# Kernel tuning notes

Measured on AMD Instinct MI355X. Metric: run time of the kernel, lower is better.

Reference implementation:

```python
import jax, jax.numpy as jnp
import numpy as np

B, T, NODES, DEG = 16, 50, 62, 8
IN, C, H, NC, K = 64, 128, 256, 3, 5
G = B * T            # num_graphs
N = G * NODES        # total nodes
E = G * NODES * DEG  # total edges (before self loops)


def setup_inputs() -> dict:
    key = jax.random.key(0)
    ks = jax.random.split(key, 12)
    # random within-graph edges, PyG-batched with node offsets
    rng = np.random.RandomState(0)
    src = rng.randint(0, NODES, size=(G, NODES * DEG))
    dst = rng.randint(0, NODES, size=(G, NODES * DEG))
    off = (np.arange(G) * NODES)[:, None]
    edge_index = jnp.asarray(np.stack([(src + off).ravel(), (dst + off).ravel()]), dtype=jnp.int32)

    def glorot(k, shape, fan_in):
        return jax.random.normal(k, shape, jnp.float32) / np.sqrt(fan_in)

    return {
        "x": jax.random.normal(ks[0], (N, IN), jnp.float32),
        "edge_index": edge_index,
        "edge_attr": jax.random.normal(ks[1], (E, 1), jnp.float32),
        "W_l": glorot(ks[2], (IN, C), IN), "b_l": jnp.zeros((C,), jnp.float32),
        "W_r": glorot(ks[3], (IN, C), IN), "b_r": jnp.zeros((C,), jnp.float32),
        "W_e": glorot(ks[4], (1, C), 1),
        "att": glorot(ks[5], (C,), C),
        "bias_out": jnp.zeros((C,), jnp.float32),
        "W_ih": glorot(ks[6], (3 * H, C), C), "W_hh": glorot(ks[7], (3 * H, H), H),
        "b_ih": jnp.zeros((3 * H,), jnp.float32), "b_hh": jnp.zeros((3 * H,), jnp.float32),
        "W1": glorot(ks[8], (H, H // 2), H), "b1": jnp.zeros((H // 2,), jnp.float32),
        "W2": glorot(ks[9], (H // 2, NC), H // 2), "b2": jnp.zeros((NC,), jnp.float32),
    }


def _forward(x, edge_index, edge_attr, W_l, b_l, W_r, b_r, W_e, att, bias_out,
             W_ih, W_hh, b_ih, b_hh, W1, b1, W2, b2):
    n = x.shape[0]
    src, dst = edge_index[0], edge_index[1]

    # --- GATv2Conv: add self loops with edge_attr fill_value='mean' (PyG default) ---
    sum_attr = jax.ops.segment_sum(edge_attr, dst, num_segments=n)
    cnt = jax.ops.segment_sum(jnp.ones_like(dst, jnp.float32), dst, num_segments=n)
    loop_attr = sum_attr / jnp.clip(cnt, 1.0)[:, None]
    ar = jnp.arange(n, dtype=src.dtype)
    src2 = jnp.concatenate([src, ar])
    dst2 = jnp.concatenate([dst, ar])
    ea = jnp.concatenate([edge_attr, loop_attr], axis=0)

    xl = x @ W_l + b_l          # source-side transform
    xr = x @ W_r + b_r          # target-side transform
    ee = ea @ W_e               # edge embedding (lin_edge, bias=False)

    m = xl[src2] + xr[dst2] + ee                # [E2, C]
    e = jax.nn.leaky_relu(m, 0.2) @ att         # [E2]
    # scatter-softmax over incoming edges per target node (self loops => no empty segs)
    emax = jax.ops.segment_max(e, dst2, num_segments=n)
    ez = jnp.exp(e - emax[dst2])
    den = jax.ops.segment_sum(ez, dst2, num_segments=n)
    alpha = ez / den[dst2]                      # [E2]
    h_sp = jax.ops.segment_sum(alpha[:, None] * xl[src2], dst2, num_segments=n) + bias_out

    # --- mean pool per graph (uniform graph size => reshape) ---
    g = h_sp.reshape(G, NODES, C).mean(axis=1).reshape(B, T, C)

    # --- GRU (PyTorch gate order r, z, n) ---
    def step(h, xt):
        gx = xt @ W_ih.T + b_ih
        gh = h @ W_hh.T + b_hh
        xr_, xz, xn = jnp.split(gx, 3, axis=-1)
        hr, hz, hn = jnp.split(gh, 3, axis=-1)
        r = jax.nn.sigmoid(xr_ + hr)
        z = jax.nn.sigmoid(xz + hz)
        nn_ = jnp.tanh(xn + r * hn)
        h2 = (1.0 - z) * nn_ + z * h
        return h2, h2

    h0 = jnp.zeros((B, H), g.dtype)
    _, hs = jax.lax.scan(step, h0, jnp.swapaxes(g, 0, 1))  # [T,B,H]
    gru_out = jnp.swapaxes(hs, 0, 1)                       # [B,T,H]

    # --- classifier (dropout inactive at eval) ---
    scores = jax.nn.relu(gru_out @ W1 + b1) @ W2 + b2      # [B,T,NC]

    # --- top-k over time per class, then mean over k ---
    vals, idx = jax.lax.top_k(jnp.swapaxes(scores, 1, 2), K)  # [B,NC,K]
    return vals.mean(axis=-1), jnp.swapaxes(idx, 1, 2)        # [B,NC], [B,K,NC]


def reference(x, edge_index, edge_attr, W_l, b_l, W_r, b_r, W_e, att, bias_out,
              W_ih, W_hh, b_ih, b_hh, W1, b1, W2, b2):
    return _forward(x, edge_index, edge_attr, W_l, b_l, W_r, b_r, W_e, att, bias_out,
                    W_ih, W_hh, b_ih, b_hh, W1, b1, W2, b2)
```

## Files before the change

### kernel.cpp

```cpp
#include <hip/hip_runtime.h>
#include <math.h>

#define NNODES 62
#define NDEG 8
#define NGRAPH 800
#define NB 16
#define NT 50
#define NIN 64
#define NCH 128
#define NH 256
#define NCLS 3
#define NTOPK 5
#define NSL 8
#define EPG (NNODES*NDEG)
#define E2G (EPG + NNODES)
#define NTOTAL (NGRAPH*NNODES)
#define ETOTAL (NGRAPH*EPG)

__launch_bounds__(256, 2)
__global__ void k_xrl(const float* __restrict__ x,
                      const float* __restrict__ W_r, const float* __restrict__ b_r,
                      const float* __restrict__ W_l, const float* __restrict__ b_l,
                      float* __restrict__ xr, float* __restrict__ xl) {
    __shared__ __align__(16) float x_s[64 * NIN];
    __shared__ __align__(16) float wr_s[NIN * NCH];
    __shared__ __align__(16) float wl_s[NIN * NCH];
    const int blk = blockIdx.x;
    const int tid = threadIdx.x;
    const int base_v = blk * 64;

    {
        const float4* src = reinterpret_cast<const float4*>(x + (size_t)base_v * NIN);
        float4* dst = reinterpret_cast<float4*>(x_s);
        for (int i = tid; i < 64 * NIN / 4; i += 256) dst[i] = src[i];
        const float4* sr = reinterpret_cast<const float4*>(W_r);
        const float4* sl = reinterpret_cast<const float4*>(W_l);
        float4* dr = reinterpret_cast<float4*>(wr_s);
        float4* dl = reinterpret_cast<float4*>(wl_s);
        for (int i = tid; i < NIN * NCH / 4; i += 256) { dr[i] = sr[i]; dl[i] = sl[i]; }
    }
    __syncthreads();

    const int c4 = (tid & 31) * 4;
    const int ng = tid >> 5;
    float4 aR[8], aL[8];
    float4 br4 = *reinterpret_cast<const float4*>(b_r + c4);
    float4 bl4 = *reinterpret_cast<const float4*>(b_l + c4);
    #pragma unroll
    for (int j = 0; j < 8; ++j) { aR[j] = br4; aL[j] = bl4; }

    const float* xs = x_s + (ng * 8) * NIN;
    for (int k4 = 0; k4 < NIN; k4 += 4) {
        float4 xv[8];
        #pragma unroll
        for (int j = 0; j < 8; ++j)
            xv[j] = *reinterpret_cast<const float4*>(&xs[j * NIN + k4]);
        #pragma unroll
        for (int kk = 0; kk < 4; ++kk) {
            float4 wr = *reinterpret_cast<const float4*>(&wr_s[(k4 + kk) * NCH + c4]);
            float4 wl = *reinterpret_cast<const float4*>(&wl_s[(k4 + kk) * NCH + c4]);
            #pragma unroll
            for (int j = 0; j < 8; ++j) {
                float xk = (kk == 0) ? xv[j].x : (kk == 1) ? xv[j].y
                         : (kk == 2) ? xv[j].z : xv[j].w;
                aR[j].x += xk * wr.x; aR[j].y += xk * wr.y;
                aR[j].z += xk * wr.z; aR[j].w += xk * wr.w;
                aL[j].x += xk * wl.x; aL[j].y += xk * wl.y;
                aL[j].z += xk * wl.z; aL[j].w += xk * wl.w;
            }
        }
    }
    #pragma unroll
    for (int j = 0; j < 8; ++j) {
        int v = base_v + ng * 8 + j;
        *reinterpret_cast<float4*>(xr + (size_t)v * NCH + c4) = aR[j];
        *reinterpret_cast<float4*>(xl + (size_t)v * NCH + c4) = aL[j];
    }
}

__global__ void k_transpose(const float* __restrict__ src, float* __restrict__ dst,
                            int rows, int cols) {
    int idx = blockIdx.x * blockDim.x + threadIdx.x;
    if (idx >= rows * cols) return;
    int r = idx / cols;
    int c = idx - r * cols;
    dst[c * rows + r] = src[idx];
}

__launch_bounds__(256, 4)
__global__ void k_gat(const int* __restrict__ ei, const float* __restrict__ eattr,
                      const float* __restrict__ W_e, const float* __restrict__ att,
                      const float* __restrict__ bias_out,
                      const float* __restrict__ xr_all, const float* __restrict__ xl_all,
                      float* __restrict__ g_all) {
    __shared__ __align__(16) float xl_s[NNODES * NCH];
    __shared__ unsigned short csr_src[E2G];
    __shared__ float csr_attr[E2G];
    __shared__ float csr_e[E2G];
    __shared__ unsigned short off_s[NNODES + 2];
    __shared__ unsigned cur_s[NNODES];
    __shared__ unsigned cnt_s[NNODES];
    __shared__ float asum_s[NNODES];
    __shared__ float la_s[NNODES];
    __shared__ float gacc_s[4 * NCH];

    const int g = blockIdx.x;
    const int tid = threadIdx.x;
    const int base_e = g * EPG;
    const int base_n = g * NNODES;

    for (int v = tid; v < NNODES; v += 256) { asum_s[v] = 0.f; cnt_s[v] = 0u; cur_s[v] = 0u; }
    {
        const float4* src = reinterpret_cast<const float4*>(xl_all + (size_t)base_n * NCH);
        float4* dst = reinterpret_cast<float4*>(xl_s);
        for (int i = tid; i < NNODES * NCH / 4; i += 256) dst[i] = src[i];
    }
    int s0 = -1, d0 = 0, s1 = -1, d1 = 0;
    float a0 = 0.f, a1 = 0.f;
    {
        int j0 = tid * 2, j1 = tid * 2 + 1;
        if (j0 < EPG) { s0 = ei[base_e + j0] - base_n; d0 = ei[ETOTAL + base_e + j0] - base_n; a0 = eattr[base_e + j0]; }
        if (j1 < EPG) { s1 = ei[base_e + j1] - base_n; d1 = ei[ETOTAL + base_e + j1] - base_n; a1 = eattr[base_e + j1]; }
    }
    __syncthreads();

    if (s0 >= 0) { atomicAdd(&cnt_s[d0], 1u); atomicAdd(&asum_s[d0], a0); }
    if (s1 >= 0) { atomicAdd(&cnt_s[d1], 1u); atomicAdd(&asum_s[d1], a1); }
    __syncthreads();

    if (tid < 64) {
        unsigned val = (tid < NNODES) ? (cnt_s[tid] + 1u) : 0u;
        unsigned xsc = val;
        #pragma unroll
        for (int dlt = 1; dlt < 64; dlt <<= 1) {
            unsigned o = __shfl_up(xsc, dlt, 64);
            if (tid >= dlt) xsc += o;
        }
        if (tid < NNODES) {
            off_s[tid] = (unsigned short)(xsc - val);
            la_s[tid] = asum_s[tid] / fmaxf((float)cnt_s[tid], 1.f);
        }
        if (tid == NNODES - 1) off_s[NNODES] = (unsigned short)xsc;
    }
    __syncthreads();

    if (s0 >= 0) { int sl = off_s[d0] + (int)atomicAdd(&cur_s[d0], 1u); csr_src[sl] = (unsigned short)s0; csr_attr[sl] = a0; }
    if (s1 >= 0) { int sl = off_s[d1] + (int)atomicAdd(&cur_s[d1], 1u); csr_src[sl] = (unsigned short)s1; csr_attr[sl] = a1; }
    if (tid < NNODES) { int sl = off_s[tid + 1] - 1; csr_src[sl] = (unsigned short)tid; csr_attr[sl] = la_s[tid]; }
    __syncthreads();

    const int wave = tid >> 6;
    const int lane = tid & 63;
    const int sub = lane & 15;
    const int gslot = wave * 4 + (lane >> 4);
    const int cb = sub * 8;

    float we0[8], at0[8];
    #pragma unroll
    for (int i = 0; i < 8; ++i) { we0[i] = W_e[cb + i]; at0[i] = att[cb + i]; }

    float acc[8];
    #pragma unroll
    for (int i = 0; i < 8; ++i) acc[i] = 0.f;

    for (int v = gslot; v < NNODES; v += 16) {
        const float* xrp = xr_all + (size_t)(base_n + v) * NCH + cb;
        float4 xr0 = *reinterpret_cast<const float4*>(xrp);
        float4 xr1 = *reinterpret_cast<const float4*>(xrp + 4);
        const int lo = off_s[v], hi = off_s[v + 1];
        float m = -INFINITY, ssum = 0.f;
        for (int sl = lo; sl < hi; ++sl) {
            int src = csr_src[sl];
            float a = csr_attr[sl];
            float4 x0 = *reinterpret_cast<const float4*>(&xl_s[src * NCH + cb]);
            float4 x1 = *reinterpret_cast<const float4*>(&xl_s[src * NCH + cb + 4]);
            float m0, t = 0.f;
            m0 = x0.x + xr0.x + a * we0[0]; t += (m0 >= 0.f ? m0 : 0.2f * m0) * at0[0];
            m0 = x0.y + xr0.y + a * we0[1]; t += (m0 >= 0.f ? m0 : 0.2f * m0) * at0[1];
            m0 = x0.z + xr0.z + a * we0[2]; t += (m0 >= 0.f ? m0 : 0.2f * m0) * at0[2];
            m0 = x0.w + xr0.w + a * we0[3]; t += (m0 >= 0.f ? m0 : 0.2f * m0) * at0[3];
            m0 = x1.x + xr1.x + a * we0[4]; t += (m0 >= 0.f ? m0 : 0.2f * m0) * at0[4];
            m0 = x1.y + xr1.y + a * we0[5]; t += (m0 >= 0.f ? m0 : 0.2f * m0) * at0[5];
            m0 = x1.z + xr1.z + a * we0[6]; t += (m0 >= 0.f ? m0 : 0.2f * m0) * at0[6];
            m0 = x1.w + xr1.w + a * we0[7]; t += (m0 >= 0.f ? m0 : 0.2f * m0) * at0[7];
            t += __shfl_xor(t, 1, 64);
            t += __shfl_xor(t, 2, 64);
            t += __shfl_xor(t, 4, 64);
            t += __shfl_xor(t, 8, 64);
            if (sub == 0) csr_e[sl] = t;
            float mn = fmaxf(m, t);
            ssum = ssum * __expf(m - mn) + __expf(t - mn);
            m = mn;
        }
        float inv = 1.f / ssum;
        for (int sl = lo; sl < hi; ++sl) {
            int src = csr_src[sl];
            float al = __expf(csr_e[sl] - m) * inv;
            float4 x0 = *reinterpret_cast<const float4*>(&xl_s[src * NCH + cb]);
            float4 x1 = *reinterpret_cast<const float4*>(&xl_s[src * NCH + cb + 4]);
            acc[0] += al * x0.x; acc[1] += al * x0.y;
            acc[2] += al * x0.z; acc[3] += al * x0.w;
            acc[4] += al * x1.x; acc[5] += al * x1.y;
            acc[6] += al * x1.z; acc[7] += al * x1.w;
        }
    }
    #pragma unroll
    for (int i = 0; i < 8; ++i) {
        acc[i] += __shfl_xor(acc[i], 16, 64);
        acc[i] += __shfl_xor(acc[i], 32, 64);
    }
    if ((lane >> 4) == 0) {
        *reinterpret_cast<float4*>(&gacc_s[wave * NCH + cb]) =
            make_float4(acc[0], acc[1], acc[2], acc[3]);
        *reinterpret_cast<float4*>(&gacc_s[wave * NCH + cb + 4]) =
            make_float4(acc[4], acc[5], acc[6], acc[7]);
    }
    __syncthreads();

    for (int c = tid; c < NCH; c += 256) {
        float v = (gacc_s[c] + gacc_s[NCH + c] + gacc_s[2 * NCH + c] + gacc_s[3 * NCH + c])
                      * (1.f / NNODES) + bias_out[c];
        g_all[(size_t)g * NCH + c] = v;
    }
}

__global__ void k_gx(const float* __restrict__ g_all, const float* __restrict__ W_ihT,
                     const float* __restrict__ b_ih, const float* __restrict__ b_hh,
                     float* __restrict__ gx_all, unsigned long long* __restrict__ h_pub) {
    if (blockIdx.x < 32)
        h_pub[(size_t)blockIdx.x * 256 + threadIdx.x] = 0ull;
    int idx = blockIdx.x * blockDim.x + threadIdx.x;
    if (idx >= NGRAPH * 3 * NH) return;
    int gi = idx / (3 * NH);
    int o = idx - gi * (3 * NH);
    float acc = b_ih[o] + (o < 2 * NH ? b_hh[o] : 0.f);
    const float* grow = g_all + (size_t)gi * NCH;
    for (int c = 0; c < NCH; ++c) acc += grow[c] * W_ihT[c * (3 * NH) + o];
    gx_all[idx] = acc;
}

__launch_bounds__(256)
__global__ void k_gru(const float* __restrict__ gx_all, const float* __restrict__ W_hh,
                      const float* __restrict__ b_hh, float* __restrict__ h_all,
                      unsigned long long* __restrict__ h_pub) {
    __shared__ __align__(16) float h_s[NH];
    __shared__ float gh_s[96];
    __shared__ float gx_s[2][96];

    const int bid = blockIdx.x;
    const int b = bid >> 3;
    const int s = bid & 7;
    const int tid = threadIdx.x;
    const int wv = tid >> 6;
    const int g = tid >> 1;
    const int l = tid & 1;

    float4 Wv[32];
    if (tid < 192) {
        int row = (g / 32) * NH + 32 * s + (g & 31);
        const float* wr = W_hh + (size_t)row * NH + 128 * l;
        #pragma unroll
        for (int j = 0; j < 32; ++j) Wv[j] = *reinterpret_cast<const float4*>(wr + 4 * j);
    }
    const float bhn = (tid < 32) ? b_hh[2 * NH + 32 * s + tid] : 0.f;
    const int own_lo = 32 * s, own_hi = own_lo + 32;

    for (int i = tid; i < NH; i += 256) h_s[i] = 0.f;
    if (wv == 3) {
        int i = tid - 192;
        int o = (i < 32) ? (32 * s + i) : (NH + 32 * s + (i - 32));
        gx_s[0][i] = gx_all[(size_t)(b * NT) * (3 * NH) + o];
        if (i < 32) gx_s[0][i + 64] = gx_all[(size_t)(b * NT) * (3 * NH) + 2 * NH + 32 * s + i];
    }
    __syncthreads();

    for (int t = 0; t < NT; ++t) {
        const int par = (t + 1) & 1;
        if (wv == 3) {
            int i = tid - 192;
            if (t + 1 < NT) {
                size_t base = (size_t)(b * NT + t + 1) * (3 * NH);
                int o = (i < 32) ? (32 * s + i) : (NH + 32 * s + (i - 32));
                gx_s[par][i] = gx_all[base + o];
                if (i < 32) gx_s[par][i + 64] = gx_all[base + 2 * NH + 32 * s + i];
            }
        } else {
            float a0 = 0.f, a1 = 0.f, a2 = 0.f, a3 = 0.f;
            #pragma unroll
            for (int j = 0; j < 32; ++j) {
                float4 hv = *reinterpret_cast<const float4*>(&h_s[128 * l + 4 * j]);
                float4 w = Wv[j];
                a0 += w.x * hv.x; a1 += w.y * hv.y; a2 += w.z * hv.z; a3 += w.w * hv.w;
            }
            float acc = (a0 + a1) + (a2 + a3);
            acc += __shfl_xor(acc, 1, 64);
            if (l == 0) gh_s[g] = acc;
        }
        __syncthreads();

        if (tid < 32) {
            const float* gx = gx_s[t & 1];
            float r = 1.f / (1.f + expf(-(gx[tid] + gh_s[tid])));
            float z = 1.f / (1.f + expf(-(gx[32 + tid] + gh_s[32 + tid])));
            float n = tanhf(gx[64 + tid] + r * (gh_s[64 + tid] + bhn));
            int o = own_lo + tid;
            float hv = (1.f - z) * n + z * h_s[o];
            h_all[(size_t)(b * NT + t) * NH + o] = hv;
            unsigned long long w = ((unsigned long long)(unsigned)(t + 1) << 32)
                                 | (unsigned long long)__float_as_uint(hv);
            __hip_atomic_store(&h_pub[((size_t)b * 2 + par) * NH + o], w,
                               __ATOMIC_RELAXED, __HIP_MEMORY_SCOPE_AGENT);
            h_s[o] = hv;
        }
        if (tid < own_lo || tid >= own_hi) {
            const unsigned long long* p = &h_pub[((size_t)b * 2 + par) * NH + tid];
            unsigned long long w;
            const unsigned target = (unsigned)(t + 1);
            while ((unsigned)((w = __hip_atomic_load(p, __ATOMIC_RELAXED,
                                                     __HIP_MEMORY_SCOPE_AGENT)) >> 32) != target)
                ;
            h_s[tid] = __uint_as_float((unsigned)w);
        }
        __syncthreads();
    }
}

__launch_bounds__(128)
__global__ void k_cls(const float* __restrict__ h_all,
                      const float* __restrict__ W1, const float* __restrict__ b1,
                      const float* __restrict__ W2, const float* __restrict__ b2,
                      float* __restrict__ sc_all) {
    __shared__ float h_s[NH];
    __shared__ float s1_s[NH / 2];
    const int bt = blockIdx.x;
    const int tid = threadIdx.x;
    h_s[tid] = h_all[(size_t)bt * NH + tid];
    h_s[tid + 128] = h_all[(size_t)bt * NH + tid + 128];
    __syncthreads();
    float acc = b1[tid];
    #pragma unroll 8
    for (int k = 0; k < NH; ++k) acc += h_s[k] * W1[k * (NH / 2) + tid];
    s1_s[tid] = fmaxf(acc, 0.f);
    __syncthreads();
    if (tid < NCLS) {
        float a = b2[tid];
        for (int k = 0; k < NH / 2; ++k) a += s1_s[k] * W2[k * NCLS + tid];
        sc_all[bt * NCLS + tid] = a;
    }
}

__global__ void k_topk(const float* __restrict__ sc_all, float* __restrict__ out) {
    int tid = threadIdx.x;
    if (tid >= NB * NCLS) return;
    int b = tid / NCLS;
    int c = tid - b * NCLS;
    float vals[NT];
    for (int t = 0; t < NT; ++t) vals[t] = sc_all[(b * NT + t) * NCLS + c];
    float sum = 0.f;
    for (int k = 0; k < NTOPK; ++k) {
        float best = -INFINITY; int bi = 0;
        for (int t = 0; t < NT; ++t) {
            if (vals[t] > best) { best = vals[t]; bi = t; }
        }
        vals[bi] = -INFINITY;
        sum += best;
        out[NB * NCLS + b * (NTOPK * NCLS) + k * NCLS + c] = (float)bi;
    }
    out[b * NCLS + c] = sum * (1.f / NTOPK);
}

extern "C" void kernel_launch(void* const* d_in, const int* in_sizes, int n_in,
                              void* d_out, int out_size, void* d_ws, size_t ws_size,
                              hipStream_t stream) {
    const float* x        = (const float*)d_in[0];
    const int*   ei       = (const int*)  d_in[1];
    const float* eattr    = (const float*)d_in[2];
    const float* W_l      = (const float*)d_in[3];
    const float* b_l      = (const float*)d_in[4];
    const float* W_r      = (const float*)d_in[5];
    const float* b_r      = (const float*)d_in[6];
    const float* W_e      = (const float*)d_in[7];
    const float* att      = (const float*)d_in[8];
    const float* bias_out = (const float*)d_in[9];
    const float* W_ih     = (const float*)d_in[10];
    const float* W_hh     = (const float*)d_in[11];
    const float* b_ih     = (const float*)d_in[12];
    const float* b_hh     = (const float*)d_in[13];
    const float* W1       = (const float*)d_in[14];
    const float* b1       = (const float*)d_in[15];
    const float* W2       = (const float*)d_in[16];
    const float* b2       = (const float*)d_in[17];
    float* out = (float*)d_out;

    float* ws = (float*)d_ws;
    float* xr_all = ws;
    float* xl_all = xr_all + (size_t)NTOTAL * NCH;
    float* g_all  = xl_all + (size_t)NTOTAL * NCH;
    float* gx_all = g_all + NGRAPH * NCH;
    float* W_ihT  = gx_all + NGRAPH * 3 * NH;
    float* h_all  = W_ihT + NCH * 3 * NH;
    float* sc_all = h_all + (size_t)NGRAPH * NH;
    unsigned long long* h_pub = (unsigned long long*)xr_all;

    k_xrl<<<NTOTAL / 64, 256, 0, stream>>>(x, W_r, b_r, W_l, b_l, xr_all, xl_all);
    k_transpose<<<(3 * NH * NCH + 255) / 256, 256, 0, stream>>>(W_ih, W_ihT, 3 * NH, NCH);
    k_gat<<<NGRAPH, 256, 0, stream>>>(ei, eattr, W_e, att, bias_out, xr_all, xl_all, g_all);
    k_gx<<<(NGRAPH * 3 * NH + 255) / 256, 256, 0, stream>>>(g_all, W_ihT, b_ih, b_hh, gx_all, h_pub);
    k_gru<<<NB * NSL, 256, 0, stream>>>(gx_all, W_hh, b_hh, h_all, h_pub);
    k_cls<<<NB * NT, 128, 0, stream>>>(h_all, W1, b1, W2, b2, sc_all);
    k_topk<<<1, 64, 0, stream>>>(sc_all, out);
}
```

Measured before the change: 227.4 us.

## Fuse node projections and W_ih transpose into GAT kernel; split GRU across more blocks

Each GAT block now computes the xl/xr projections for its own graph directly into padded shared memory, using 512 threads. This removes the separate projection kernel and the global round-trip of the xr/xl arrays. The W_ih transpose is folded into extra trailing blocks of the same launch, and the GRU recurrence is spread over 16 slices per batch with 4 lanes per gate row instead of 8 slices. The fused kernel reloads W_r/W_l into shared memory in every block and uses a large shared footprint, which limits occupancy to one block. The finer GRU split also adds more cross-block spin synchronization per step.

```diff
diff --git a/kernel.cpp b/kernel.cpp
--- a/kernel.cpp
+++ b/kernel.cpp
@@ -11,121 +11,116 @@
 #define NH 256
 #define NCLS 3
 #define NTOPK 5
-#define NSL 8
+#define NSL 16
 #define EPG (NNODES*NDEG)
 #define E2G (EPG + NNODES)
 #define NTOTAL (NGRAPH*NNODES)
 #define ETOTAL (NGRAPH*EPG)
-
-__launch_bounds__(256, 2)
-__global__ void k_xrl(const float* __restrict__ x,
+#define TBLK 97
+#define WST (NIN*NCH + 4)
+#define XST 68
+#define XLST 132
+
+__launch_bounds__(512, 1)
+__global__ void k_gat(const float* __restrict__ x, const int* __restrict__ ei,
+                      const float* __restrict__ eattr,
                       const float* __restrict__ W_r, const float* __restrict__ b_r,
                       const float* __restrict__ W_l, const float* __restrict__ b_l,
-                      float* __restrict__ xr, float* __restrict__ xl) {
-    __shared__ __align__(16) float x_s[64 * NIN];
-    __shared__ __align__(16) float wr_s[NIN * NCH];
-    __shared__ __align__(16) float wl_s[NIN * NCH];
-    const int blk = blockIdx.x;
-    const int tid = threadIdx.x;
-    const int base_v = blk * 64;
-
-    {
-        const float4* src = reinterpret_cast<const float4*>(x + (size_t)base_v * NIN);
-        float4* dst = reinterpret_cast<float4*>(x_s);
-        for (int i = tid; i < 64 * NIN / 4; i += 256) dst[i] = src[i];
-        const float4* sr = reinterpret_cast<const float4*>(W_r);
-        const float4* sl = reinterpret_cast<const float4*>(W_l);
-        float4* dr = reinterpret_cast<float4*>(wr_s);
-        float4* dl = reinterpret_cast<float4*>(wl_s);
-        for (int i = tid; i < NIN * NCH / 4; i += 256) { dr[i] = sr[i]; dl[i] = sl[i]; }
-    }
-    __syncthreads();
-
-    const int c4 = (tid & 31) * 4;
-    const int ng = tid >> 5;
-    float4 aR[8], aL[8];
-    float4 br4 = *reinterpret_cast<const float4*>(b_r + c4);
-    float4 bl4 = *reinterpret_cast<const float4*>(b_l + c4);
-    #pragma unroll
-    for (int j = 0; j < 8; ++j) { aR[j] = br4; aL[j] = bl4; }
-
-    const float* xs = x_s + (ng * 8) * NIN;
-    for (int k4 = 0; k4 < NIN; k4 += 4) {
-        float4 xv[8];
-        #pragma unroll
-        for (int j = 0; j < 8; ++j)
-            xv[j] = *reinterpret_cast<const float4*>(&xs[j * NIN + k4]);
-        #pragma unroll
-        for (int kk = 0; kk < 4; ++kk) {
-            float4 wr = *reinterpret_cast<const float4*>(&wr_s[(k4 + kk) * NCH + c4]);
-            float4 wl = *reinterpret_cast<const float4*>(&wl_s[(k4 + kk) * NCH + c4]);
-            #pragma unroll
-            for (int j = 0; j < 8; ++j) {
-                float xk = (kk == 0) ? xv[j].x : (kk == 1) ? xv[j].y
-                         : (kk == 2) ? xv[j].z : xv[j].w;
-                aR[j].x += xk * wr.x; aR[j].y += xk * wr.y;
-                aR[j].z += xk * wr.z; aR[j].w += xk * wr.w;
-                aL[j].x += xk * wl.x; aL[j].y += xk * wl.y;
-                aL[j].z += xk * wl.z; aL[j].w += xk * wl.w;
-            }
-        }
-    }
-    #pragma unroll
-    for (int j = 0; j < 8; ++j) {
-        int v = base_v + ng * 8 + j;
-        *reinterpret_cast<float4*>(xr + (size_t)v * NCH + c4) = aR[j];
-        *reinterpret_cast<float4*>(xl + (size_t)v * NCH + c4) = aL[j];
-    }
-}
-
-__global__ void k_transpose(const float* __restrict__ src, float* __restrict__ dst,
-                            int rows, int cols) {
-    int idx = blockIdx.x * blockDim.x + threadIdx.x;
-    if (idx >= rows * cols) return;
-    int r = idx / cols;
-    int c = idx - r * cols;
-    dst[c * rows + r] = src[idx];
-}
-
-__launch_bounds__(256, 4)
-__global__ void k_gat(const int* __restrict__ ei, const float* __restrict__ eattr,
                       const float* __restrict__ W_e, const float* __restrict__ att,
                       const float* __restrict__ bias_out,
-                      const float* __restrict__ xr_all, const float* __restrict__ xl_all,
+                      const float* __restrict__ W_ih, float* __restrict__ W_ihT,
                       float* __restrict__ g_all) {
-    __shared__ __align__(16) float xl_s[NNODES * NCH];
-    __shared__ unsigned short csr_src[E2G];
+    __shared__ __align__(16) float w_s[2 * WST];
+    __shared__ __align__(16) float x_s[64 * XST];
+    __shared__ __align__(16) float xl_s[NNODES * XLST];
+    __shared__ __align__(16) float xr_s[NNODES * XLST];
     __shared__ float csr_attr[E2G];
     __shared__ float csr_e[E2G];
+    __shared__ unsigned short csr_src[E2G];
     __shared__ unsigned short off_s[NNODES + 2];
     __shared__ unsigned cur_s[NNODES];
     __shared__ unsigned cnt_s[NNODES];
     __shared__ float asum_s[NNODES];
     __shared__ float la_s[NNODES];
-    __shared__ float gacc_s[4 * NCH];
+    __shared__ float gacc_s[8 * NCH];
 
     const int g = blockIdx.x;
     const int tid = threadIdx.x;
+    if (g >= NGRAPH) {
+        for (int idx = (g - NGRAPH) * 512 + tid; idx < 3 * NH * NCH; idx += TBLK * 512) {
+            int r = idx / NCH, c = idx - r * NCH;
+            W_ihT[c * (3 * NH) + r] = W_ih[idx];
+        }
+        return;
+    }
     const int base_e = g * EPG;
     const int base_n = g * NNODES;
 
-    for (int v = tid; v < NNODES; v += 256) { asum_s[v] = 0.f; cnt_s[v] = 0u; cur_s[v] = 0u; }
+    for (int v = tid; v < NNODES; v += 512) { asum_s[v] = 0.f; cnt_s[v] = 0u; cur_s[v] = 0u; }
+    int s0 = -1, d0 = 0; float a0e = 0.f;
+    if (tid < EPG) {
+        s0 = ei[base_e + tid] - base_n;
+        d0 = ei[ETOTAL + base_e + tid] - base_n;
+        a0e = eattr[base_e + tid];
+    }
     {
-        const float4* src = reinterpret_cast<const float4*>(xl_all + (size_t)base_n * NCH);
-        float4* dst = reinterpret_cast<float4*>(xl_s);
-        for (int i = tid; i < NNODES * NCH / 4; i += 256) dst[i] = src[i];
-    }
-    int s0 = -1, d0 = 0, s1 = -1, d1 = 0;
-    float a0 = 0.f, a1 = 0.f;
-    {
-        int j0 = tid * 2, j1 = tid * 2 + 1;
-        if (j0 < EPG) { s0 = ei[base_e + j0] - base_n; d0 = ei[ETOTAL + base_e + j0] - base_n; a0 = eattr[base_e + j0]; }
-        if (j1 < EPG) { s1 = ei[base_e + j1] - base_n; d1 = ei[ETOTAL + base_e + j1] - base_n; a1 = eattr[base_e + j1]; }
-    }
-    __syncthreads();
-
-    if (s0 >= 0) { atomicAdd(&cnt_s[d0], 1u); atomicAdd(&asum_s[d0], a0); }
-    if (s1 >= 0) { atomicAdd(&cnt_s[d1], 1u); atomicAdd(&asum_s[d1], a1); }
+        float4* dr = reinterpret_cast<float4*>(w_s);
+        float4* dl = reinterpret_cast<float4*>(w_s + WST);
+        const float4* sr = reinterpret_cast<const float4*>(W_r);
+        const float4* sl = reinterpret_cast<const float4*>(W_l);
+        for (int i = tid; i < NIN * NCH / 4; i += 512) { dr[i] = sr[i]; dl[i] = sl[i]; }
+        for (int i = tid; i < NNODES * (NIN / 4); i += 512) {
+            int r = i >> 4, c = i & 15;
+            reinterpret_cast<float4*>(&x_s[r * XST])[c] =
+                reinterpret_cast<const float4*>(x + (size_t)(base_n + r) * NIN)[c];
+        }
+    }
+    __syncthreads();
+    if (s0 >= 0) { atomicAdd(&cnt_s[d0], 1u); atomicAdd(&asum_s[d0], a0e); }
+
+    if (tid < 256) {
+        const int mat = tid >> 7;
+        const int u = tid & 127;
+        const int cg = u & 15;
+        const int ng = u >> 4;
+        const int cb2 = cg * 8;
+        const float* Ws = w_s + mat * WST;
+        const float* bb = mat ? b_l : b_r;
+        float4 bv0 = *reinterpret_cast<const float4*>(bb + cb2);
+        float4 bv1 = *reinterpret_cast<const float4*>(bb + cb2 + 4);
+        float4 A0[8], A1[8];
+        #pragma unroll
+        for (int j = 0; j < 8; ++j) { A0[j] = bv0; A1[j] = bv1; }
+        for (int k4 = 0; k4 < NIN; k4 += 4) {
+            float4 xv[8];
+            #pragma unroll
+            for (int j = 0; j < 8; ++j)
+                xv[j] = *reinterpret_cast<const float4*>(&x_s[(ng * 8 + j) * XST + k4]);
+            #pragma unroll
+            for (int kk = 0; kk < 4; ++kk) {
+                float4 w0 = *reinterpret_cast<const float4*>(&Ws[(k4 + kk) * NCH + cb2]);
+                float4 w1 = *reinterpret_cast<const float4*>(&Ws[(k4 + kk) * NCH + cb2 + 4]);
+                #pragma unroll
+                for (int j = 0; j < 8; ++j) {
+                    float xk = (kk == 0) ? xv[j].x : (kk == 1) ? xv[j].y
+                             : (kk == 2) ? xv[j].z : xv[j].w;
+                    A0[j].x += xk * w0.x; A0[j].y += xk * w0.y;
+                    A0[j].z += xk * w0.z; A0[j].w += xk * w0.w;
+                    A1[j].x += xk * w1.x; A1[j].y += xk * w1.y;
+                    A1[j].z += xk * w1.z; A1[j].w += xk * w1.w;
+                }
+            }
+        }
+        float* dst = mat ? xl_s : xr_s;
+        #pragma unroll
+        for (int j = 0; j < 8; ++j) {
+            int v = ng * 8 + j;
+            if (v < NNODES) {
+                *reinterpret_cast<float4*>(&dst[v * XLST + cb2]) = A0[j];
+                *reinterpret_cast<float4*>(&dst[v * XLST + cb2 + 4]) = A1[j];
+            }
+        }
+    }
     __syncthreads();
 
     if (tid < 64) {
@@ -143,10 +138,14 @@
         if (tid == NNODES - 1) off_s[NNODES] = (unsigned short)xsc;
     }
     __syncthreads();
-
-    if (s0 >= 0) { int sl = off_s[d0] + (int)atomicAdd(&cur_s[d0], 1u); csr_src[sl] = (unsigned short)s0; csr_attr[sl] = a0; }
-    if (s1 >= 0) { int sl = off_s[d1] + (int)atomicAdd(&cur_s[d1], 1u); csr_src[sl] = (unsigned short)s1; csr_attr[sl] = a1; }
-    if (tid < NNODES) { int sl = off_s[tid + 1] - 1; csr_src[sl] = (unsigned short)tid; csr_attr[sl] = la_s[tid]; }
+    if (s0 >= 0) {
+        int sl = off_s[d0] + (int)atomicAdd(&cur_s[d0], 1u);
+        csr_src[sl] = (unsigned short)s0; csr_attr[sl] = a0e;
+    }
+    if (tid < NNODES) {
+        int sl = off_s[tid + 1] - 1;
+        csr_src[sl] = (unsigned short)tid; csr_attr[sl] = la_s[tid];
+    }
     __syncthreads();
 
     const int wave = tid >> 6;
@@ -154,35 +153,32 @@
     const int sub = lane & 15;
     const int gslot = wave * 4 + (lane >> 4);
     const int cb = sub * 8;
-
     float we0[8], at0[8];
     #pragma unroll
     for (int i = 0; i < 8; ++i) { we0[i] = W_e[cb + i]; at0[i] = att[cb + i]; }
-
     float acc[8];
     #pragma unroll
     for (int i = 0; i < 8; ++i) acc[i] = 0.f;
 
-    for (int v = gslot; v < NNODES; v += 16) {
-        const float* xrp = xr_all + (size_t)(base_n + v) * NCH + cb;
-        float4 xr0 = *reinterpret_cast<const float4*>(xrp);
-        float4 xr1 = *reinterpret_cast<const float4*>(xrp + 4);
+    for (int v = gslot; v < NNODES; v += 32) {
+        float4 xr0 = *reinterpret_cast<const float4*>(&xr_s[v * XLST + cb]);
+        float4 xr1 = *reinterpret_cast<const float4*>(&xr_s[v * XLST + cb + 4]);
         const int lo = off_s[v], hi = off_s[v + 1];
         float m = -INFINITY, ssum = 0.f;
         for (int sl = lo; sl < hi; ++sl) {
             int src = csr_src[sl];
             float a = csr_attr[sl];
-            float4 x0 = *reinterpret_cast<const float4*>(&xl_s[src * NCH + cb]);
-            float4 x1 = *reinterpret_cast<const float4*>(&xl_s[src * NCH + cb + 4]);
-            float m0, t = 0.f;
-            m0 = x0.x + xr0.x + a * we0[0]; t += (m0 >= 0.f ? m0 : 0.2f * m0) * at0[0];
-            m0 = x0.y + xr0.y + a * we0[1]; t += (m0 >= 0.f ? m0 : 0.2f * m0) * at0[1];
-            m0 = x0.z + xr0.z + a * we0[2]; t += (m0 >= 0.f ? m0 : 0.2f * m0) * at0[2];
-            m0 = x0.w + xr0.w + a * we0[3]; t += (m0 >= 0.f ? m0 : 0.2f * m0) * at0[3];
-            m0 = x1.x + xr1.x + a * we0[4]; t += (m0 >= 0.f ? m0 : 0.2f * m0) * at0[4];
-            m0 = x1.y + xr1.y + a * we0[5]; t += (m0 >= 0.f ? m0 : 0.2f * m0) * at0[5];
-            m0 = x1.z + xr1.z + a * we0[6]; t += (m0 >= 0.f ? m0 : 0.2f * m0) * at0[6];
-            m0 = x1.w + xr1.w + a * we0[7]; t += (m0 >= 0.f ? m0 : 0.2f * m0) * at0[7];
+            float4 x0 = *reinterpret_cast<const float4*>(&xl_s[src * XLST + cb]);
+            float4 x1 = *reinterpret_cast<const float4*>(&xl_s[src * XLST + cb + 4]);
+            float mi, t = 0.f;
+            mi = x0.x + xr0.x + a * we0[0]; t += (mi >= 0.f ? mi : 0.2f * mi) * at0[0];
+            mi = x0.y + xr0.y + a * we0[1]; t += (mi >= 0.f ? mi : 0.2f * mi) * at0[1];
+            mi = x0.z + xr0.z + a * we0[2]; t += (mi >= 0.f ? mi : 0.2f * mi) * at0[2];
+            mi = x0.w + xr0.w + a * we0[3]; t += (mi >= 0.f ? mi : 0.2f * mi) * at0[3];
+            mi = x1.x + xr1.x + a * we0[4]; t += (mi >= 0.f ? mi : 0.2f * mi) * at0[4];
+            mi = x1.y + xr1.y + a * we0[5]; t += (mi >= 0.f ? mi : 0.2f * mi) * at0[5];
+            mi = x1.z + xr1.z + a * we0[6]; t += (mi >= 0.f ? mi : 0.2f * mi) * at0[6];
+            mi = x1.w + xr1.w + a * we0[7]; t += (mi >= 0.f ? mi : 0.2f * mi) * at0[7];
             t += __shfl_xor(t, 1, 64);
             t += __shfl_xor(t, 2, 64);
             t += __shfl_xor(t, 4, 64);
@@ -196,8 +192,8 @@
         for (int sl = lo; sl < hi; ++sl) {
             int src = csr_src[sl];
             float al = __expf(csr_e[sl] - m) * inv;
-            float4 x0 = *reinterpret_cast<const float4*>(&xl_s[src * NCH + cb]);
-            float4 x1 = *reinterpret_cast<const float4*>(&xl_s[src * NCH + cb + 4]);
+            float4 x0 = *reinterpret_cast<const float4*>(&xl_s[src * XLST + cb]);
+            float4 x1 = *reinterpret_cast<const float4*>(&xl_s[src * XLST + cb + 4]);
             acc[0] += al * x0.x; acc[1] += al * x0.y;
             acc[2] += al * x0.z; acc[3] += al * x0.w;
             acc[4] += al * x1.x; acc[5] += al * x1.y;
@@ -217,10 +213,11 @@
     }
     __syncthreads();
 
-    for (int c = tid; c < NCH; c += 256) {
-        float v = (gacc_s[c] + gacc_s[NCH + c] + gacc_s[2 * NCH + c] + gacc_s[3 * NCH + c])
-                      * (1.f / NNODES) + bias_out[c];
-        g_all[(size_t)g * NCH + c] = v;
+    for (int c = tid; c < NCH; c += 512) {
+        float vsum = 0.f;
+        #pragma unroll
+        for (int w = 0; w < 8; ++w) vsum += gacc_s[w * NCH + c];
+        g_all[(size_t)g * NCH + c] = vsum * (1.f / NNODES) + bias_out[c];
     }
 }
 
@@ -244,65 +241,73 @@
                       const float* __restrict__ b_hh, float* __restrict__ h_all,
                       unsigned long long* __restrict__ h_pub) {
     __shared__ __align__(16) float h_s[NH];
-    __shared__ float gh_s[96];
-    __shared__ float gx_s[2][96];
+    __shared__ float gh_s[48];
+    __shared__ float gx_s[2][48];
 
     const int bid = blockIdx.x;
-    const int b = bid >> 3;
-    const int s = bid & 7;
+    const int b = bid >> 4;
+    const int s = bid & 15;
     const int tid = threadIdx.x;
     const int wv = tid >> 6;
-    const int g = tid >> 1;
-    const int l = tid & 1;
-
-    float4 Wv[32];
+    const int g = tid >> 2;
+    const int l = tid & 3;
+
+    float4 Wv[16];
     if (tid < 192) {
-        int row = (g / 32) * NH + 32 * s + (g & 31);
-        const float* wr = W_hh + (size_t)row * NH + 128 * l;
+        int row = (g < 16) ? (NSL * s + g)
+                : (g < 32) ? (NH + NSL * s + (g - 16))
+                           : (2 * NH + NSL * s + (g - 32));
+        const float* wr = W_hh + (size_t)row * NH + 64 * l;
         #pragma unroll
-        for (int j = 0; j < 32; ++j) Wv[j] = *reinterpret_cast<const float4*>(wr + 4 * j);
-    }
-    const float bhn = (tid < 32) ? b_hh[2 * NH + 32 * s + tid] : 0.f;
-    const int own_lo = 32 * s, own_hi = own_lo + 32;
+        for (int j = 0; j < 16; ++j) {
+            int jeff = (j + 2 * l) & 15;
+            Wv[j] = *reinterpret_cast<const float4*>(wr + 4 * jeff);
+        }
+    }
+    const float bhn = (tid < NSL) ? b_hh[2 * NH + NSL * s + tid] : 0.f;
+    const int own_lo = NSL * s, own_hi = NSL * s + NSL;
 
     for (int i = tid; i < NH; i += 256) h_s[i] = 0.f;
     if (wv == 3) {
         int i = tid - 192;
-        int o = (i < 32) ? (32 * s + i) : (NH + 32 * s + (i - 32));
-        gx_s[0][i] = gx_all[(size_t)(b * NT) * (3 * NH) + o];
-        if (i < 32) gx_s[0][i + 64] = gx_all[(size_t)(b * NT) * (3 * NH) + 2 * NH + 32 * s + i];
+        if (i < 48) {
+            int o = (i < 16) ? (NSL * s + i) : (i < 32) ? (NH + NSL * s + i - 16)
+                                                        : (2 * NH + NSL * s + i - 32);
+            gx_s[0][i] = gx_all[(size_t)(b * NT + 0) * (3 * NH) + o];
+        }
     }
     __syncthreads();
 
     for (int t = 0; t < NT; ++t) {
-        const int par = (t + 1) & 1;
         if (wv == 3) {
             int i = tid - 192;
-            if (t + 1 < NT) {
-                size_t base = (size_t)(b * NT + t + 1) * (3 * NH);
-                int o = (i < 32) ? (32 * s + i) : (NH + 32 * s + (i - 32));
-                gx_s[par][i] = gx_all[base + o];
-                if (i < 32) gx_s[par][i + 64] = gx_all[base + 2 * NH + 32 * s + i];
+            if (i < 48 && t + 1 < NT) {
+                int o = (i < 16) ? (NSL * s + i) : (i < 32) ? (NH + NSL * s + i - 16)
+                                                            : (2 * NH + NSL * s + i - 32);
+                gx_s[(t + 1) & 1][i] = gx_all[(size_t)(b * NT + t + 1) * (3 * NH) + o];
             }
         } else {
             float a0 = 0.f, a1 = 0.f, a2 = 0.f, a3 = 0.f;
             #pragma unroll
-            for (int j = 0; j < 32; ++j) {
-                float4 hv = *reinterpret_cast<const float4*>(&h_s[128 * l + 4 * j]);
+            for (int j = 0; j < 16; ++j) {
+                int jeff = (j + 2 * l) & 15;
+                float4 hv = *reinterpret_cast<const float4*>(&h_s[64 * l + 4 * jeff]);
                 float4 w = Wv[j];
                 a0 += w.x * hv.x; a1 += w.y * hv.y; a2 += w.z * hv.z; a3 += w.w * hv.w;
             }
             float acc = (a0 + a1) + (a2 + a3);
             acc += __shfl_xor(acc, 1, 64);
+            acc += __shfl_xor(acc, 2, 64);
             if (l == 0) gh_s[g] = acc;
         }
         __syncthreads();
 
-        if (tid < 32) {
+        const int par = (t + 1) & 1;
+        if (tid < NSL) {
             const float* gx = gx_s[t & 1];
             float r = 1.f / (1.f + expf(-(gx[tid] + gh_s[tid])));
-            float z = 1.f / (1.f + expf(-(gx[32 + tid] + gh_s[32 + tid])));
-            float n = tanhf(gx[64 + tid] + r * (gh_s[64 + tid] + bhn));
+            float z = 1.f / (1.f + expf(-(gx[16 + tid] + gh_s[16 + tid])));
+            float n = tanhf(gx[32 + tid] + r * (gh_s[32 + tid] + bhn));
             int o = own_lo + tid;
             float hv = (1.f - z) * n + z * h_s[o];
             h_all[(size_t)(b * NT + t) * NH + o] = hv;
@@ -393,19 +398,17 @@
     float* out = (float*)d_out;
 
     float* ws = (float*)d_ws;
-    float* xr_all = ws;
-    float* xl_all = xr_all + (size_t)NTOTAL * NCH;
-    float* g_all  = xl_all + (size_t)NTOTAL * NCH;
+    float* g_all  = ws;
     float* gx_all = g_all + NGRAPH * NCH;
     float* W_ihT  = gx_all + NGRAPH * 3 * NH;
     float* h_all  = W_ihT + NCH * 3 * NH;
     float* sc_all = h_all + (size_t)NGRAPH * NH;
-    unsigned long long* h_pub = (unsigned long long*)xr_all;
-
-    k_xrl<<<NTOTAL / 64, 256, 0, stream>>>(x, W_r, b_r, W_l, b_l, xr_all, xl_all);
-    k_transpose<<<(3 * NH * NCH + 255) / 256, 256, 0, stream>>>(W_ih, W_ihT, 3 * NH, NCH);
-    k_gat<<<NGRAPH, 256, 0, stream>>>(ei, eattr, W_e, att, bias_out, xr_all, xl_all, g_all);
-    k_gx<<<(NGRAPH * 3 * NH + 255) / 256, 256, 0, stream>>>(g_all, W_ihT, b_ih, b_hh, gx_all, h_pub);
+    unsigned long long* h_pub = (unsigned long long*)(sc_all + NGRAPH * NCLS);
+
+    k_gat<<<NGRAPH + TBLK, 512, 0, stream>>>(x, ei, eattr, W_r, b_r, W_l, b_l,
+                                             W_e, att, bias_out, W_ih, W_ihT, g_all);
+    k_gx<<<(NGRAPH * 3 * NH + 255) / 256, 256, 0, stream>>>(g_all, W_ihT, b_ih, b_hh,
+                                                            gx_all, h_pub);
     k_gru<<<NB * NSL, 256, 0, stream>>>(gx_all, W_hh, b_hh, h_all, h_pub);
     k_cls<<<NB * NT, 128, 0, stream>>>(h_all, W1, b1, W2, b2, sc_all);
     k_topk<<<1, 64, 0, stream>>>(sc_all, out);
```

New measurement: 238.5 us. 1.05x slower.

## Run each GRU batch row in one 768-thread block, drop cross-block spin sync

Applied to the files above, without the earlier changes.

The GRU recurrence used to split each batch row across 8 blocks that swapped hidden-state slices every timestep through agent-scope atomic publish and spin-wait. Now one 768-thread block per batch row holds the full W_hh in registers, one row per thread, and syncs only with __syncthreads. This removes inter-block polling latency and the h_pub zeroing in k_gx. In exchange, only 16 blocks run, each thread needs 256 floats of weights in registers (likely spills at 768 threads), the per-thread dot product is a long serial chain, and the gx prefetch is gone.

```diff
diff --git a/kernel.cpp b/kernel.cpp
--- a/kernel.cpp
+++ b/kernel.cpp
@@ -11,7 +11,6 @@
 #define NH 256
 #define NCLS 3
 #define NTOPK 5
-#define NSL 8
 #define EPG (NNODES*NDEG)
 #define E2G (EPG + NNODES)
 #define NTOTAL (NGRAPH*NNODES)
@@ -174,15 +173,15 @@
             float a = csr_attr[sl];
             float4 x0 = *reinterpret_cast<const float4*>(&xl_s[src * NCH + cb]);
             float4 x1 = *reinterpret_cast<const float4*>(&xl_s[src * NCH + cb + 4]);
-            float m0, t = 0.f;
-            m0 = x0.x + xr0.x + a * we0[0]; t += (m0 >= 0.f ? m0 : 0.2f * m0) * at0[0];
-            m0 = x0.y + xr0.y + a * we0[1]; t += (m0 >= 0.f ? m0 : 0.2f * m0) * at0[1];
-            m0 = x0.z + xr0.z + a * we0[2]; t += (m0 >= 0.f ? m0 : 0.2f * m0) * at0[2];
-            m0 = x0.w + xr0.w + a * we0[3]; t += (m0 >= 0.f ? m0 : 0.2f * m0) * at0[3];
-            m0 = x1.x + xr1.x + a * we0[4]; t += (m0 >= 0.f ? m0 : 0.2f * m0) * at0[4];
-            m0 = x1.y + xr1.y + a * we0[5]; t += (m0 >= 0.f ? m0 : 0.2f * m0) * at0[5];
-            m0 = x1.z + xr1.z + a * we0[6]; t += (m0 >= 0.f ? m0 : 0.2f * m0) * at0[6];
-            m0 = x1.w + xr1.w + a * we0[7]; t += (m0 >= 0.f ? m0 : 0.2f * m0) * at0[7];
+            float mi, t = 0.f;
+            mi = x0.x + xr0.x + a * we0[0]; t += (mi >= 0.f ? mi : 0.2f * mi) * at0[0];
+            mi = x0.y + xr0.y + a * we0[1]; t += (mi >= 0.f ? mi : 0.2f * mi) * at0[1];
+            mi = x0.z + xr0.z + a * we0[2]; t += (mi >= 0.f ? mi : 0.2f * mi) * at0[2];
+            mi = x0.w + xr0.w + a * we0[3]; t += (mi >= 0.f ? mi : 0.2f * mi) * at0[3];
+            mi = x1.x + xr1.x + a * we0[4]; t += (mi >= 0.f ? mi : 0.2f * mi) * at0[4];
+            mi = x1.y + xr1.y + a * we0[5]; t += (mi >= 0.f ? mi : 0.2f * mi) * at0[5];
+            mi = x1.z + xr1.z + a * we0[6]; t += (mi >= 0.f ? mi : 0.2f * mi) * at0[6];
+            mi = x1.w + xr1.w + a * we0[7]; t += (mi >= 0.f ? mi : 0.2f * mi) * at0[7];
             t += __shfl_xor(t, 1, 64);
             t += __shfl_xor(t, 2, 64);
             t += __shfl_xor(t, 4, 64);
@@ -226,9 +225,7 @@
 
 __global__ void k_gx(const float* __restrict__ g_all, const float* __restrict__ W_ihT,
                      const float* __restrict__ b_ih, const float* __restrict__ b_hh,
-                     float* __restrict__ gx_all, unsigned long long* __restrict__ h_pub) {
-    if (blockIdx.x < 32)
-        h_pub[(size_t)blockIdx.x * 256 + threadIdx.x] = 0ull;
+                     float* __restrict__ gx_all) {
     int idx = blockIdx.x * blockDim.x + threadIdx.x;
     if (idx >= NGRAPH * 3 * NH) return;
     int gi = idx / (3 * NH);
@@ -239,87 +236,49 @@
     gx_all[idx] = acc;
 }
 
-__launch_bounds__(256)
+__launch_bounds__(768, 1)
 __global__ void k_gru(const float* __restrict__ gx_all, const float* __restrict__ W_hh,
-                      const float* __restrict__ b_hh, float* __restrict__ h_all,
-                      unsigned long long* __restrict__ h_pub) {
+                      const float* __restrict__ b_hh, float* __restrict__ h_all) {
     __shared__ __align__(16) float h_s[NH];
-    __shared__ float gh_s[96];
-    __shared__ float gx_s[2][96];
-
-    const int bid = blockIdx.x;
-    const int b = bid >> 3;
-    const int s = bid & 7;
+    __shared__ float gh_s[3 * NH];
+
+    const int b = blockIdx.x;
     const int tid = threadIdx.x;
-    const int wv = tid >> 6;
-    const int g = tid >> 1;
-    const int l = tid & 1;
-
-    float4 Wv[32];
-    if (tid < 192) {
-        int row = (g / 32) * NH + 32 * s + (g & 31);
-        const float* wr = W_hh + (size_t)row * NH + 128 * l;
-        #pragma unroll
-        for (int j = 0; j < 32; ++j) Wv[j] = *reinterpret_cast<const float4*>(wr + 4 * j);
-    }
-    const float bhn = (tid < 32) ? b_hh[2 * NH + 32 * s + tid] : 0.f;
-    const int own_lo = 32 * s, own_hi = own_lo + 32;
-
-    for (int i = tid; i < NH; i += 256) h_s[i] = 0.f;
-    if (wv == 3) {
-        int i = tid - 192;
-        int o = (i < 32) ? (32 * s + i) : (NH + 32 * s + (i - 32));
-        gx_s[0][i] = gx_all[(size_t)(b * NT) * (3 * NH) + o];
-        if (i < 32) gx_s[0][i + 64] = gx_all[(size_t)(b * NT) * (3 * NH) + 2 * NH + 32 * s + i];
-    }
+
+    float4 Wv[64];
+    {
+        const float* wr = W_hh + (size_t)tid * NH;
+        #pragma unroll
+        for (int j = 0; j < 64; ++j)
+            Wv[j] = *reinterpret_cast<const float4*>(wr + 4 * j);
+    }
+    const float bhn = (tid < NH) ? b_hh[2 * NH + tid] : 0.f;
+
+    if (tid < NH) h_s[tid] = 0.f;
     __syncthreads();
 
     for (int t = 0; t < NT; ++t) {
-        const int par = (t + 1) & 1;
-        if (wv == 3) {
-            int i = tid - 192;
-            if (t + 1 < NT) {
-                size_t base = (size_t)(b * NT + t + 1) * (3 * NH);
-                int o = (i < 32) ? (32 * s + i) : (NH + 32 * s + (i - 32));
-                gx_s[par][i] = gx_all[base + o];
-                if (i < 32) gx_s[par][i + 64] = gx_all[base + 2 * NH + 32 * s + i];
-            }
-        } else {
-            float a0 = 0.f, a1 = 0.f, a2 = 0.f, a3 = 0.f;
-            #pragma unroll
-            for (int j = 0; j < 32; ++j) {
-                float4 hv = *reinterpret_cast<const float4*>(&h_s[128 * l + 4 * j]);
-                float4 w = Wv[j];
-                a0 += w.x * hv.x; a1 += w.y * hv.y; a2 += w.z * hv.z; a3 += w.w * hv.w;
-            }
-            float acc = (a0 + a1) + (a2 + a3);
-            acc += __shfl_xor(acc, 1, 64);
-            if (l == 0) gh_s[g] = acc;
-        }
+        float gxr = 0.f, gxz = 0.f, gxn = 0.f;
+        if (tid < NH) {
+            const float* gx = gx_all + (size_t)(b * NT + t) * (3 * NH);
+            gxr = gx[tid]; gxz = gx[tid + NH]; gxn = gx[tid + 2 * NH];
+        }
+        float acc = 0.f;
+        #pragma unroll
+        for (int j = 0; j < 64; ++j) {
+            float4 hv = *reinterpret_cast<const float4*>(&h_s[4 * j]);
+            acc += hv.x * Wv[j].x + hv.y * Wv[j].y + hv.z * Wv[j].z + hv.w * Wv[j].w;
+        }
+        gh_s[tid] = acc;
         __syncthreads();
 
-        if (tid < 32) {
-            const float* gx = gx_s[t & 1];
-            float r = 1.f / (1.f + expf(-(gx[tid] + gh_s[tid])));
-            float z = 1.f / (1.f + expf(-(gx[32 + tid] + gh_s[32 + tid])));
-            float n = tanhf(gx[64 + tid] + r * (gh_s[64 + tid] + bhn));
-            int o = own_lo + tid;
-            float hv = (1.f - z) * n + z * h_s[o];
-            h_all[(size_t)(b * NT + t) * NH + o] = hv;
-            unsigned long long w = ((unsigned long long)(unsigned)(t + 1) << 32)
-                                 | (unsigned long long)__float_as_uint(hv);
-            __hip_atomic_store(&h_pub[((size_t)b * 2 + par) * NH + o], w,
-                               __ATOMIC_RELAXED, __HIP_MEMORY_SCOPE_AGENT);
-            h_s[o] = hv;
-        }
-        if (tid < own_lo || tid >= own_hi) {
-            const unsigned long long* p = &h_pub[((size_t)b * 2 + par) * NH + tid];
-            unsigned long long w;
-            const unsigned target = (unsigned)(t + 1);
-            while ((unsigned)((w = __hip_atomic_load(p, __ATOMIC_RELAXED,
-                                                     __HIP_MEMORY_SCOPE_AGENT)) >> 32) != target)
-                ;
-            h_s[tid] = __uint_as_float((unsigned)w);
+        if (tid < NH) {
+            float r = 1.f / (1.f + expf(-(gxr + gh_s[tid])));
+            float z = 1.f / (1.f + expf(-(gxz + gh_s[tid + NH])));
+            float n = tanhf(gxn + r * (gh_s[tid + 2 * NH] + bhn));
+            float hv = (1.f - z) * n + z * h_s[tid];
+            h_s[tid] = hv;
+            h_all[(size_t)(b * NT + t) * NH + tid] = hv;
         }
         __syncthreads();
     }
@@ -400,13 +359,12 @@
     float* W_ihT  = gx_all + NGRAPH * 3 * NH;
     float* h_all  = W_ihT + NCH * 3 * NH;
     float* sc_all = h_all + (size_t)NGRAPH * NH;
-    unsigned long long* h_pub = (unsigned long long*)xr_all;
 
     k_xrl<<<NTOTAL / 64, 256, 0, stream>>>(x, W_r, b_r, W_l, b_l, xr_all, xl_all);
     k_transpose<<<(3 * NH * NCH + 255) / 256, 256, 0, stream>>>(W_ih, W_ihT, 3 * NH, NCH);
     k_gat<<<NGRAPH, 256, 0, stream>>>(ei, eattr, W_e, att, bias_out, xr_all, xl_all, g_all);
-    k_gx<<<(NGRAPH * 3 * NH + 255) / 256, 256, 0, stream>>>(g_all, W_ihT, b_ih, b_hh, gx_all, h_pub);
-    k_gru<<<NB * NSL, 256, 0, stream>>>(gx_all, W_hh, b_hh, h_all, h_pub);
+    k_gx<<<(NGRAPH * 3 * NH + 255) / 256, 256, 0, stream>>>(g_all, W_ihT, b_ih, b_hh, gx_all);
+    k_gru<<<NB, 768, 0, stream>>>(gx_all, W_hh, b_hh, h_all);
     k_cls<<<NB * NT, 128, 0, stream>>>(h_all, W1, b1, W2, b2, sc_all);
     k_topk<<<1, 64, 0, stream>>>(sc_all, out);
 }
```

Result: slower. 730.8 us (+221.4%).
